# Optimization experiments

Measured on AMD Instinct MI355X. Metric: run time of the kernel, lower is better.

Reference implementation:

```python
import jax, jax.numpy as jnp
import numpy as np

# Dimensions matching init_kwargs
B, S, D, d_feat, O = 64, 1024, 64, 2, 10
L = S // 2  # label_site
STD = 0.01  # 'random_eye' init noise scale


def setup_inputs() -> dict:
    key = jax.random.key(0)
    k1, k2, k3, k4 = jax.random.split(key, 4)
    x = jax.random.normal(k1, (B, S, d_feat), dtype=jnp.float32)
    # InputRegion tensors, bond_str 'slri': eye over (l, r) broadcast over (s, i)
    W_left = jnp.eye(D, dtype=jnp.float32)[None, :, :, None] \
        + STD * jax.random.normal(k2, (L, D, D, d_feat), dtype=jnp.float32)
    W_right = jnp.eye(D, dtype=jnp.float32)[None, :, :, None] \
        + STD * jax.random.normal(k3, (S - L, D, D, d_feat), dtype=jnp.float32)
    # OutputSite tensor, bond_str 'olr': eye over (l, r) broadcast over o
    out_core = jnp.eye(D, dtype=jnp.float32)[None, :, :] \
        + STD * jax.random.normal(k4, (O, D, D), dtype=jnp.float32)
    return {"x": x, "W_left": W_left, "out_core": out_core, "W_right": W_right}


def reference(x, W_left, out_core, W_right):
    # x: [B, S, d]; W_left: [L, D, D, d]; out_core: [O, D, D]; W_right: [S-L, D, D, d]
    Ls = W_left.shape[0]
    Dv = W_left.shape[1]
    Bv = x.shape[0]
    # Per-site matrices (einsum 'slri,bsi->bslr'), laid out scan-major [S, B, D, D]
    mats_l = jnp.einsum('slri,bsi->sblr', W_left, x[:, :Ls])
    mats_r = jnp.einsum('slri,bsi->sblr', W_right, x[:, Ls:])
    # Open boundary edge vectors e = [1, 0, ..., 0]
    e = jnp.zeros((Dv,), dtype=x.dtype).at[0].set(1.0)
    v0 = jnp.broadcast_to(e, (Bv, Dv))
    # Left-to-right vector propagation through left chain
    def lstep(v, m):
        return jnp.einsum('bl,blr->br', v, m), None
    vL, _ = jax.lax.scan(lstep, v0, mats_l)
    # Right-to-left vector propagation through right chain
    def rstep(w, m):
        return jnp.einsum('blr,br->bl', m, w), None
    wR, _ = jax.lax.scan(rstep, v0, mats_r, reverse=True)
    # Contract through the output core: [B, O]
    return jnp.einsum('bl,olr,br->bo', vL, out_core, wR)
```

## Files before the change

kernel.cpp:

```cpp
#include <hip/hip_runtime.h>
#include <stdint.h>

#define NSITE 512
#define DD    64
#define NB    64
#define NO    10
#define NSEG  16
#define SEGLEN 32
#define SLAB_BYTES 32768
#define PACK_BYTES 16384
#define WS_NEED (2u * NSITE * SLAB_BYTES)

typedef short bf16x8 __attribute__((ext_vector_type(8)));
typedef float f32x16 __attribute__((ext_vector_type(16)));

__device__ __forceinline__ uint32_t pk2(float a, float b) {
    return __builtin_amdgcn_perm(__float_as_uint(b), __float_as_uint(a), 0x07060302);
}

__device__ __forceinline__ float2 pkmul2(float2 a, float2 b) {
    float2 r;
    asm("v_pk_mul_f32 %0, %1, %2" : "=v"(r) : "v"(a), "v"(b));
    return r;
}

__global__ __launch_bounds__(256) void pack_kernel(const float* wlsrc,
                                                   const float* wrsrc,
                                                   char* dl, char* dr) {
    const int g = blockIdx.x;
    const int right = (g >= NSITE) ? 1 : 0;
    const int s = right ? g - NSITE : g;
    const float* src = (right ? wrsrc : wlsrc) + (size_t)s * (SLAB_BYTES / 4);
    char* dst = (right ? dr : dl) + (size_t)s * SLAB_BYTES;

    __shared__ float2 st[DD * 65];
    const float4* src4 = (const float4*)src;
    for (int e4 = threadIdx.x; e4 < DD * DD / 2; e4 += 256) {
        const float4 v = src4[e4];
        const int e = e4 * 2;
        float2* d = &st[(e >> 6) * 65 + (e & 63)];
        d[0] = make_float2(v.x, v.y);
        d[1] = make_float2(v.z, v.w);
    }
    __syncthreads();

    uint32_t* out = (uint32_t*)dst;
    #pragma unroll
    for (int rr = 0; rr < 16; ++rr) {
        const int od = rr * 256 + threadIdx.x;
        const int chunk = od >> 8, i = chunk >> 3, sk = chunk & 7;
        const int H = (od >> 7) & 1, m5 = (od >> 2) & 31, d = od & 3;
        const int m = 32 * i + m5, k = 8 * sk + 4 * H + d;
        const float2 a = right ? st[m * 65 + k] : st[k * 65 + m];
        out[od] = pk2(a.x, a.y);
    }
}

__device__ __forceinline__ void dma16(const void* gp, void* lp) {
    __builtin_amdgcn_global_load_lds(
        (const __attribute__((address_space(1))) uint32_t*)gp,
        (__attribute__((address_space(3))) uint32_t*)lp, 16, 0, 0);
}

__global__ __launch_bounds__(256, 3) void stage1_kernel(
        const float* __restrict__ x, char* __restrict__ dl, char* __restrict__ dr) {
    const int pb   = blockIdx.x;
    const int bid  = (pb & 7) * 64 + (pb >> 3);
    const int side = bid >> 8;
    const int seg  = (bid >> 4) & 15;
    const int bq   = bid & 15;
    const int wave = threadIdx.x >> 6;
    const int lane = threadIdx.x & 63;
    const int b    = bq * 4 + wave;
    const int m5   = lane & 31;
    const int H    = lane >> 5;

    __shared__ __align__(16) char ring[3][PACK_BYTES];
    __shared__ float2 xs[4][SEGLEN];

    char* wbuf = side ? dr : dl;

    if (lane < SEGLEN) {
        const float2* xp = ((const float2*)x) + (size_t)b * 1024 + (side ? NSITE : 0);
        const int sg = seg * SEGLEN + (side ? SEGLEN - 1 - lane : lane);
        xs[wave][lane] = xp[sg];
    }

    auto siteAddr = [&](int t) -> const char* {
        const int sg = seg * SEGLEN + (side ? SEGLEN - 1 - t : t);
        return wbuf + (size_t)sg * SLAB_BYTES;
    };

    #pragma unroll
    for (int t0 = 0; t0 < 2; ++t0) {
        const char* sb = siteAddr(t0);
        #pragma unroll
        for (int c = 0; c < 4; ++c) {
            const int ch = wave * 4 + c;
            dma16(sb + ch * 1024 + lane * 16, ring[t0] + ch * 1024);
        }
    }

    f32x16 acc[2][2];
    #pragma unroll
    for (int i = 0; i < 2; ++i)
        #pragma unroll
        for (int j = 0; j < 2; ++j)
            #pragma unroll
            for (int q = 0; q < 16; ++q) {
                const int row = (q & 3) + 8 * (q >> 2) + 4 * H;
                acc[i][j][q] = (i == j && row == m5) ? 1.f : 0.f;
            }

    f32x16 zf;
    #pragma unroll
    for (int q = 0; q < 16; ++q) zf[q] = 0.f;

    union BU { bf16x8 v; uint32_t w[4]; };

    int cur = 0;
    for (int t = 0; t < SEGLEN; ++t) {
        asm volatile("s_waitcnt vmcnt(4)" ::: "memory");
        asm volatile("s_barrier" ::: "memory");

        {
            int t2 = t + 2; if (t2 > SEGLEN - 1) t2 = SEGLEN - 1;
            int ns = cur + 2; if (ns >= 3) ns -= 3;
            const char* sb = siteAddr(t2);
            char* lb = ring[ns];
            #pragma unroll
            for (int c = 0; c < 4; ++c) {
                const int ch = wave * 4 + c;
                dma16(sb + ch * 1024 + lane * 16, lb + ch * 1024);
            }
        }

        const char* rb = ring[cur];
        const float2 xv = xs[wave][t];
        const float2 xx = make_float2(xv.x, xv.x);
        const float2 xy = make_float2(xv.y, xv.y);

        BU bfa[8][2];
        #pragma unroll
        for (int sk = 0; sk < 8; ++sk) {
            const int mi = sk >> 2, qb = 4 * (sk & 3);
            #pragma unroll
            for (int j = 0; j < 2; ++j)
                #pragma unroll
                for (int dp = 0; dp < 2; ++dp) {
                    const float2 v01 = make_float2(acc[mi][j][qb + 2 * dp],
                                                   acc[mi][j][qb + 2 * dp + 1]);
                    const float2 pa = pkmul2(xx, v01);
                    const float2 pb = pkmul2(xy, v01);
                    bfa[sk][j].w[2 * dp + 0] = pk2(pa.x, pb.x);
                    bfa[sk][j].w[2 * dp + 1] = pk2(pa.y, pb.y);
                }
        }

        __builtin_amdgcn_s_setprio(1);
        #pragma unroll
        for (int sk = 0; sk < 8; ++sk) {
            #pragma unroll
            for (int i = 0; i < 2; ++i) {
                union { bf16x8 v; uint4 u; } a;
                a.u = *(const uint4*)(rb + (i * 8 + sk) * 1024 + lane * 16);
                #pragma unroll
                for (int j = 0; j < 2; ++j)
                    acc[i][j] = __builtin_amdgcn_mfma_f32_32x32x16_bf16(
                        a.v, bfa[sk][j].v, (sk == 0) ? zf : acc[i][j], 0, 0, 0);
            }
        }
        __builtin_amdgcn_s_setprio(0);

        ++cur; if (cur >= 3) cur -= 3;
    }

    {
        const int p = b * NSEG + seg;
        char* pdst = wbuf + (size_t)(p >> 1) * SLAB_BYTES + PACK_BYTES + (p & 1) * 8192;
        #pragma unroll
        for (int i = 0; i < 2; ++i)
            #pragma unroll
            for (int j = 0; j < 2; ++j) {
                const int c = 32 * j + m5;
                #pragma unroll
                for (int Q = 0; Q < 4; ++Q) {
                    const int r0 = 32 * i + 8 * Q + 4 * H;
                    uint2 val;
                    val.x = pk2(acc[i][j][4 * Q + 0], acc[i][j][4 * Q + 1]);
                    val.y = pk2(acc[i][j][4 * Q + 2], acc[i][j][4 * Q + 3]);
                    *(uint2*)(pdst + c * 128 + r0 * 2) = val;
                }
            }
    }
    asm volatile("s_waitcnt vmcnt(0)" ::: "memory");
}

__global__ __launch_bounds__(512) void tail_kernel(
        const char* __restrict__ dl, const char* __restrict__ dr,
        const float* __restrict__ core, float* __restrict__ out) {
    const int b    = blockIdx.x;
    const int tid  = threadIdx.x;
    const int side = tid >> 8;
    const int r    = tid & 63;
    const int cg   = (tid >> 6) & 3;
    const char* wbuf = side ? dr : dl;

    __shared__ float vsh[2][DD];
    __shared__ float part[2][4][DD];
    if ((tid & 255) < DD) vsh[side][r] = (r == 0) ? 1.f : 0.f;

    auto Pseg = [&](int gi) -> const uint16_t* {
        const int g = side ? (NSEG - 1 - gi) : gi;
        const int p = b * NSEG + g;
        return (const uint16_t*)(wbuf
            + (size_t)(p >> 1) * SLAB_BYTES + PACK_BYTES + (p & 1) * 8192);
    };

    float pv[16];
    {
        const uint16_t* P = Pseg(0);
        #pragma unroll
        for (int cc = 0; cc < 16; ++cc)
            pv[cc] = __uint_as_float(((uint32_t)P[(cg * 16 + cc) * 64 + r]) << 16);
    }
    __syncthreads();

    for (int gi = 0; gi < NSEG; ++gi) {
        float nv[16];
        const bool more = (gi + 1 < NSEG);
        if (more) {
            const uint16_t* Pn = Pseg(gi + 1);
            #pragma unroll
            for (int cc = 0; cc < 16; ++cc)
                nv[cc] = __uint_as_float(((uint32_t)Pn[(cg * 16 + cc) * 64 + r]) << 16);
        }
        float acc = 0.f;
        #pragma unroll
        for (int cc = 0; cc < 16; ++cc)
            acc = fmaf(vsh[side][cg * 16 + cc], pv[cc], acc);
        part[side][cg][r] = acc;
        asm volatile("s_waitcnt lgkmcnt(0)" ::: "memory");
        __builtin_amdgcn_s_barrier();
        if ((tid & 255) < DD)
            vsh[side][r] = part[side][0][r] + part[side][1][r]
                         + part[side][2][r] + part[side][3][r];
        asm volatile("s_waitcnt lgkmcnt(0)" ::: "memory");
        __builtin_amdgcn_s_barrier();
        if (more) {
            #pragma unroll
            for (int cc = 0; cc < 16; ++cc) pv[cc] = nv[cc];
        }
    }
    const int wv   = tid >> 6;
    const int lane = tid & 63;
    const float wrv = vsh[1][lane];
    for (int o = wv; o < NO; o += 8) {
        float acc = 0.f;
        #pragma unroll 8
        for (int l = 0; l < DD; ++l)
            acc += vsh[0][l] * core[(o * DD + l) * DD + lane];
        acc *= wrv;
        #pragma unroll
        for (int off = 32; off > 0; off >>= 1)
            acc += __shfl_xor(acc, off, 64);
        if (lane == 0) out[b * NO + o] = acc;
    }
}

extern "C" void kernel_launch(void* const* d_in, const int* in_sizes, int n_in,
                              void* d_out, int out_size, void* d_ws, size_t ws_size,
                              hipStream_t stream) {
    const float* x    = (const float*)d_in[0];
    float*       wl   = (float*)d_in[1];
    const float* core = (const float*)d_in[2];
    float*       wr   = (float*)d_in[3];

    char* dl;
    char* dr;
    if (ws_size >= (size_t)WS_NEED) {
        dl = (char*)d_ws;
        dr = dl + (size_t)NSITE * SLAB_BYTES;
    } else {
        dl = (char*)wl;
        dr = (char*)wr;
    }

    pack_kernel<<<2 * NSITE, 256, 0, stream>>>(wl, wr, dl, dr);
    stage1_kernel<<<512, 256, 0, stream>>>(x, dl, dr);
    tail_kernel<<<NB, 512, 0, stream>>>(dl, dr, core, (float*)d_out);
}
```

Baseline: 161.7 us.

## Use one-wave blocks in stage1 with per-wave double-buffered site loads

Stage1 moves from 256-thread blocks, where four waves share each site slab through a 3-deep LDS ring and a block barrier, to 64-thread single-wave blocks. Each wave streams all 16 chunks of every site slab itself into a 2-slot ring, so the s_barrier is gone. The wave reads the whole A fragment into registers before reusing that slot for the next DMA, and it takes x through a wave shuffle instead of LDS. The intent is to drop inter-wave synchronisation and let blocks schedule independently. The cost is that the same weight slabs are now fetched once per batch row instead of once per four, roughly quadrupling global/L2 traffic, and af[2][8] adds register pressure.

Measured after the change: 208.7 us. 1.29x slower.

```diff
diff --git a/kernel.cpp b/kernel.cpp
--- a/kernel.cpp
+++ b/kernel.cpp
@@ -62,28 +62,26 @@
         (__attribute__((address_space(3))) uint32_t*)lp, 16, 0, 0);
 }
 
-__global__ __launch_bounds__(256, 3) void stage1_kernel(
+__global__ __launch_bounds__(64, 2) void stage1_kernel(
         const float* __restrict__ x, char* __restrict__ dl, char* __restrict__ dr) {
     const int pb   = blockIdx.x;
-    const int bid  = (pb & 7) * 64 + (pb >> 3);
-    const int side = bid >> 8;
-    const int seg  = (bid >> 4) & 15;
-    const int bq   = bid & 15;
-    const int wave = threadIdx.x >> 6;
-    const int lane = threadIdx.x & 63;
-    const int b    = bq * 4 + wave;
+    const int bid  = (pb & 7) * 256 + (pb >> 3);
+    const int side = bid >> 10;
+    const int seg  = (bid >> 6) & 15;
+    const int b    = bid & 63;
+    const int lane = threadIdx.x;
     const int m5   = lane & 31;
     const int H    = lane >> 5;
 
-    __shared__ __align__(16) char ring[3][PACK_BYTES];
-    __shared__ float2 xs[4][SEGLEN];
+    __shared__ __align__(16) char ring[2][PACK_BYTES];
 
     char* wbuf = side ? dr : dl;
 
+    float2 xreg = make_float2(0.f, 0.f);
     if (lane < SEGLEN) {
         const float2* xp = ((const float2*)x) + (size_t)b * 1024 + (side ? NSITE : 0);
         const int sg = seg * SEGLEN + (side ? SEGLEN - 1 - lane : lane);
-        xs[wave][lane] = xp[sg];
+        xreg = xp[sg];
     }
 
     auto siteAddr = [&](int t) -> const char* {
@@ -95,10 +93,8 @@
     for (int t0 = 0; t0 < 2; ++t0) {
         const char* sb = siteAddr(t0);
         #pragma unroll
-        for (int c = 0; c < 4; ++c) {
-            const int ch = wave * 4 + c;
-            dma16(sb + ch * 1024 + lane * 16, ring[t0] + ch * 1024);
-        }
+        for (int c = 0; c < 16; ++c)
+            dma16(sb + c * 1024 + lane * 16, ring[t0] + c * 1024);
     }
 
     f32x16 acc[2][2];
@@ -118,32 +114,39 @@
 
     union BU { bf16x8 v; uint32_t w[4]; };
 
-    int cur = 0;
     for (int t = 0; t < SEGLEN; ++t) {
-        asm volatile("s_waitcnt vmcnt(4)" ::: "memory");
-        asm volatile("s_barrier" ::: "memory");
+        asm volatile("s_waitcnt vmcnt(16)" ::: "memory");
+        __builtin_amdgcn_sched_barrier(0);
+
+        const char* rb = ring[t & 1];
+        uint4 af[2][8];
+        #pragma unroll
+        for (int i = 0; i < 2; ++i)
+            #pragma unroll
+            for (int sk = 0; sk < 8; ++sk)
+                af[i][sk] = *(const uint4*)(rb + (i * 8 + sk) * 1024 + lane * 16);
+        __builtin_amdgcn_sched_barrier(0);
+        asm volatile("s_waitcnt lgkmcnt(0)" ::: "memory");
+        __builtin_amdgcn_sched_barrier(0);
 
         {
             int t2 = t + 2; if (t2 > SEGLEN - 1) t2 = SEGLEN - 1;
-            int ns = cur + 2; if (ns >= 3) ns -= 3;
             const char* sb = siteAddr(t2);
-            char* lb = ring[ns];
-            #pragma unroll
-            for (int c = 0; c < 4; ++c) {
-                const int ch = wave * 4 + c;
-                dma16(sb + ch * 1024 + lane * 16, lb + ch * 1024);
-            }
-        }
-
-        const char* rb = ring[cur];
-        const float2 xv = xs[wave][t];
+            char* lb = ring[t & 1];
+            #pragma unroll
+            for (int c = 0; c < 16; ++c)
+                dma16(sb + c * 1024 + lane * 16, lb + c * 1024);
+        }
+
+        const float2 xv = make_float2(__shfl(xreg.x, t, 64), __shfl(xreg.y, t, 64));
         const float2 xx = make_float2(xv.x, xv.x);
         const float2 xy = make_float2(xv.y, xv.y);
 
-        BU bfa[8][2];
+        __builtin_amdgcn_s_setprio(1);
         #pragma unroll
         for (int sk = 0; sk < 8; ++sk) {
             const int mi = sk >> 2, qb = 4 * (sk & 3);
+            BU bfa[2];
             #pragma unroll
             for (int j = 0; j < 2; ++j)
                 #pragma unroll
@@ -152,27 +155,19 @@
                                                    acc[mi][j][qb + 2 * dp + 1]);
                     const float2 pa = pkmul2(xx, v01);
                     const float2 pb = pkmul2(xy, v01);
-                    bfa[sk][j].w[2 * dp + 0] = pk2(pa.x, pb.x);
-                    bfa[sk][j].w[2 * dp + 1] = pk2(pa.y, pb.y);
+                    bfa[j].w[2 * dp + 0] = pk2(pa.x, pb.x);
+                    bfa[j].w[2 * dp + 1] = pk2(pa.y, pb.y);
                 }
-        }
-
-        __builtin_amdgcn_s_setprio(1);
-        #pragma unroll
-        for (int sk = 0; sk < 8; ++sk) {
             #pragma unroll
             for (int i = 0; i < 2; ++i) {
-                union { bf16x8 v; uint4 u; } a;
-                a.u = *(const uint4*)(rb + (i * 8 + sk) * 1024 + lane * 16);
+                union { bf16x8 v; uint4 u; } a; a.u = af[i][sk];
                 #pragma unroll
                 for (int j = 0; j < 2; ++j)
                     acc[i][j] = __builtin_amdgcn_mfma_f32_32x32x16_bf16(
-                        a.v, bfa[sk][j].v, (sk == 0) ? zf : acc[i][j], 0, 0, 0);
+                        a.v, bfa[j].v, (sk == 0) ? zf : acc[i][j], 0, 0, 0);
             }
         }
         __builtin_amdgcn_s_setprio(0);
-
-        ++cur; if (cur >= 3) cur -= 3;
     }
 
     {
@@ -287,6 +282,6 @@
     }
 
     pack_kernel<<<2 * NSITE, 256, 0, stream>>>(wl, wr, dl, dr);
-    stage1_kernel<<<512, 256, 0, stream>>>(x, dl, dr);
+    stage1_kernel<<<2048, 64, 0, stream>>>(x, dl, dr);
     tail_kernel<<<NB, 512, 0, stream>>>(dl, dr, core, (float*)d_out);
 }
```
